# Kernel optimization log

Hardware: AMD Instinct MI355X
Metric: run time of the kernel (lower is better)

The kernel has to match this reference:

```python
import jax, jax.numpy as jnp
import numpy as np

B, S, D = 2, 2048, 2048
H, KV, HD = 32, 8, 64          # n_heads, n_kv_heads, head_dim
NREP = H // KV                 # GQA repeat factor
ROPE_THETA = 500000.0          # llama3 base


def setup_inputs() -> dict:
    key = jax.random.key(0)
    ks = jax.random.split(key, 5)
    scale = 1.0 / np.sqrt(D)
    x = jax.random.normal(ks[0], (B, S, D), dtype=jnp.float32)
    wq = jax.random.normal(ks[1], (D, H * HD), dtype=jnp.float32) * scale
    wk = jax.random.normal(ks[2], (D, KV * HD), dtype=jnp.float32) * scale
    wv = jax.random.normal(ks[3], (D, KV * HD), dtype=jnp.float32) * scale
    wo = jax.random.normal(ks[4], (H * HD, D), dtype=jnp.float32) * scale
    # real rotary freqs, matching precompute_freqs_cis: angle[t, j] = t / theta^(2j/HD)
    inv_freq = 1.0 / (ROPE_THETA ** (np.arange(0, HD, 2, dtype=np.float32) / HD))
    t = np.arange(S, dtype=np.float32)
    ang = np.outer(t, inv_freq)  # (S, HD//2)
    freqs_cos = jnp.asarray(np.cos(ang), dtype=jnp.float32)
    freqs_sin = jnp.asarray(np.sin(ang), dtype=jnp.float32)
    return {"x": x, "wq": wq, "wk": wk, "wv": wv, "wo": wo,
            "freqs_cos": freqs_cos, "freqs_sin": freqs_sin}


def _apply_rope(t, cos, sin):
    # t: (B, S, nh, HD); pairs (even, odd) = (real, imag) of complex number
    tr = t.reshape(*t.shape[:-1], HD // 2, 2)
    re, im = tr[..., 0], tr[..., 1]
    c = cos[None, :, None, :]   # (1, S, 1, HD//2)
    s = sin[None, :, None, :]
    out_re = re * c - im * s
    out_im = re * s + im * c
    return jnp.stack([out_re, out_im], axis=-1).reshape(t.shape)


def reference(x, wq, wk, wv, wo, freqs_cos, freqs_sin):
    bsz, seq_len, _ = x.shape
    xq = (x @ wq).reshape(bsz, seq_len, H, HD)
    xk = (x @ wk).reshape(bsz, seq_len, KV, HD)
    xv = (x @ wv).reshape(bsz, seq_len, KV, HD)
    xq = _apply_rope(xq, freqs_cos, freqs_sin)
    xk = _apply_rope(xk, freqs_cos, freqs_sin)
    # GQA without materializing repeated KV: group query heads by KV head
    q = xq.transpose(0, 2, 1, 3).reshape(bsz, KV, NREP, seq_len, HD)  # bgrqh
    k = xk.transpose(0, 2, 1, 3)                                      # bgkh over seq k
    v = xv.transpose(0, 2, 1, 3)
    scores = jnp.einsum("bgrqh,bgkh->bgrqk", q, k) / jnp.sqrt(jnp.float32(HD))
    causal = jnp.tril(jnp.ones((seq_len, seq_len), dtype=bool))
    scores = jnp.where(causal[None, None, None], scores, -jnp.inf)
    probs = jax.nn.softmax(scores.astype(jnp.float32), axis=-1).astype(q.dtype)
    out = jnp.einsum("bgrqk,bgkh->bgrqh", probs, v)
    out = out.reshape(bsz, H, seq_len, HD).transpose(0, 2, 1, 3).reshape(bsz, seq_len, H * HD)
    return out @ wo
```

## Files before the change

kernel.cpp:

```cpp
#include <hip/hip_runtime.h>
#include <hip/hip_bf16.h>

typedef __attribute__((ext_vector_type(8))) short bf16x8;
typedef __attribute__((ext_vector_type(4))) float f32x4;
typedef __attribute__((ext_vector_type(16))) float f32x16;

#define S_LEN 2048
#define DMODEL 2048
#define NH 32
#define NKV 8
#define HDIM 64
#define NQKV 3072
#define BROWS 4096
#define LOG2E 1.4426950408889634f

__device__ __forceinline__ float bf2f(unsigned short u) {
    union { unsigned int i; float f; } v; v.i = ((unsigned int)u) << 16; return v.f;
}
__device__ __forceinline__ unsigned short f2bf(float f) {
    union { float f; unsigned int i; } v; v.f = f;
    unsigned int r = v.i + 0x7fffu + ((v.i >> 16) & 1u);
    return (unsigned short)(r >> 16);
}

__device__ __forceinline__ unsigned cvtpk_bf16(float lo, float hi) {
    unsigned r;
    asm("v_cvt_pk_bf16_f32 %0, %1, %2" : "=v"(r) : "v"(lo), "v"(hi));
    return r;
}
__device__ __forceinline__ void pl32swap(unsigned &a, unsigned &b) {
    asm("v_permlane32_swap_b32 %0, %1" : "+v"(a), "+v"(b));
}
__device__ __forceinline__ float exp2_fast(float x) {
    float r;
    asm("v_exp_f32 %0, %1" : "=v"(r) : "v"(x));
    return r;
}

__device__ __forceinline__ void gload_lds16(const void* g, void* l) {
    __builtin_amdgcn_global_load_lds(
        (const __attribute__((address_space(1))) unsigned int*)(unsigned long long)g,
        (__attribute__((address_space(3))) unsigned int*)(unsigned int)(unsigned long long)l,
        16, 0, 0);
}

#define VMW(n) asm volatile("s_waitcnt vmcnt(" #n ")" ::: "memory")
#define CFENCE() asm volatile("" ::: "memory")

__global__ void cast_x_kernel(const float* __restrict__ x, unsigned short* __restrict__ xb) {
    int idx = blockIdx.x * blockDim.x + threadIdx.x;
    float4 v = ((const float4*)x)[idx];
    ushort4 o;
    o.x = f2bf(v.x); o.y = f2bf(v.y); o.z = f2bf(v.z); o.w = f2bf(v.w);
    ((ushort4*)xb)[idx] = o;
}

__global__ void tcast_kernel(const float* __restrict__ src, unsigned short* __restrict__ dst,
                             int K, int N) {
    __shared__ float t[32][33];
    int n0 = blockIdx.x * 32, k0 = blockIdx.y * 32;
    int tx = threadIdx.x & 31, ty = threadIdx.x >> 5;
#pragma unroll
    for (int i = 0; i < 32; i += 8)
        t[ty + i][tx] = src[(size_t)(k0 + ty + i) * N + n0 + tx];
    __syncthreads();
#pragma unroll
    for (int i = 0; i < 32; i += 8)
        dst[(size_t)(n0 + ty + i) * K + k0 + tx] = f2bf(t[tx][ty + i]);
}

__global__ void vtrans_kernel(const unsigned short* __restrict__ qkv,
                              unsigned short* __restrict__ vt) {
    __shared__ unsigned short t[32][33];
    int s0 = blockIdx.x * 32;
    int hd0 = (blockIdx.y & 1) * 32;
    int bg = blockIdx.y >> 1;
    int b = bg >> 3, g = bg & 7;
    int tx = threadIdx.x & 31, ty = threadIdx.x >> 5;
#pragma unroll
    for (int i = 0; i < 32; i += 8)
        t[ty + i][tx] = qkv[(size_t)(b * S_LEN + s0 + ty + i) * NQKV + 2560 + g * 64 + hd0 + tx];
    __syncthreads();
#pragma unroll
    for (int i = 0; i < 32; i += 8)
        vt[(size_t)(bg * 64 + hd0 + ty + i) * S_LEN + s0 + tx] = t[tx][ty + i];
}

template <int NJF, int OUTF32>
__global__ __launch_bounds__(512, 2) void gemm_wide_kernel(
    const unsigned short* __restrict__ A,
    const unsigned short* __restrict__ BT,
    void* __restrict__ Cv,
    int M, int N, int K, int nbx) {
    extern __shared__ __align__(16) unsigned short lds[];
    const int ABUF = 8192;
    const int BSTRIDE = NJF * 4096;
    const int BBASE = 2 * ABUF;

    const int nwg = gridDim.x;
    const int cpx = nwg >> 3;
    const int swz = ((int)blockIdx.x & 7) * cpx + ((int)blockIdx.x >> 3);
    const int m0 = (swz / nbx) * 128, n0 = (swz % nbx) * (NJF * 64);

    const int tid = threadIdx.x;
    const int lane = tid & 63, wid = tid >> 6;
    const int wr = wid >> 2, wc = wid & 3;
    const int l16 = lane & 15, lg = lane >> 4;

    const int sr0 = tid >> 3, sk0 = tid & 7;
    const int kc = (sk0 ^ (sr0 & 7)) * 8;
    const size_t K64 = (size_t)64 * K;
    const unsigned short* gA = A + (size_t)(m0 + sr0) * K + kc;
    const unsigned short* gB = BT + (size_t)(n0 + sr0) * K + kc;
    unsigned short* ldsA = lds + tid * 8;
    unsigned short* ldsB = lds + BBASE + tid * 8;

    f32x4 acc[4][NJF];
#pragma unroll
    for (int i = 0; i < 4; ++i)
#pragma unroll
        for (int j = 0; j < NJF; ++j)
#pragma unroll
            for (int e = 0; e < 4; ++e) acc[i][j][e] = 0.f;

    const int NT = K >> 6;
    {
        gload_lds16(gA, ldsA);
        gload_lds16(gA + K64, ldsA + 4096);
#pragma unroll
        for (int j = 0; j < NJF; ++j)
            gload_lds16(gB + (size_t)j * K64, ldsB + j * 4096);
    }

    for (int t = 0; t < NT; ++t) {
        const int cur = t & 1, nxt = cur ^ 1;
        if (t + 1 < NT) {
            gload_lds16(gA + 64, ldsA + nxt * ABUF);
            gload_lds16(gA + 64 + K64, ldsA + nxt * ABUF + 4096);
#pragma unroll
            for (int j = 0; j < NJF; ++j)
                gload_lds16(gB + 64 + (size_t)j * K64, ldsB + nxt * BSTRIDE + j * 4096);
            if constexpr (NJF == 6) { VMW(8); } else { VMW(6); }
        } else {
            VMW(0);
        }
        __builtin_amdgcn_s_barrier();
        CFENCE();

#pragma unroll
        for (int ks = 0; ks < 2; ++ks) {
            bf16x8 af[4], bfv[NJF];
#pragma unroll
            for (int mi = 0; mi < 4; ++mi) {
                const int rA = wr * 64 + mi * 16 + l16;
                af[mi] = *(const bf16x8*)(lds + cur * ABUF + rA * 64 + ((ks * 4 + lg) ^ (rA & 7)) * 8);
            }
#pragma unroll
            for (int nj = 0; nj < NJF; ++nj) {
                const int rB = nj * 64 + wc * 16 + l16;
                bfv[nj] = *(const bf16x8*)(lds + BBASE + cur * BSTRIDE + rB * 64 + ((ks * 4 + lg) ^ (rB & 7)) * 8);
            }
#pragma unroll
            for (int mi = 0; mi < 4; ++mi)
#pragma unroll
                for (int nj = 0; nj < NJF; ++nj)
                    acc[mi][nj] = __builtin_amdgcn_mfma_f32_16x16x32_bf16(
                        af[mi], bfv[nj], acc[mi][nj], 0, 0, 0);
        }
        CFENCE();
        __builtin_amdgcn_s_barrier();
        CFENCE();
        gA += 64;
        gB += 64;
    }

#pragma unroll
    for (int mi = 0; mi < 4; ++mi) {
        const int row = m0 + wr * 64 + mi * 16 + lg * 4;
#pragma unroll
        for (int e = 0; e < 4; ++e) {
            if (OUTF32) {
                float* Cf = (float*)Cv;
#pragma unroll
                for (int nj = 0; nj < NJF; ++nj)
                    Cf[(size_t)(row + e) * N + n0 + nj * 64 + wc * 16 + l16] = acc[mi][nj][e];
            } else {
                unsigned short* Cb = (unsigned short*)Cv;
#pragma unroll
                for (int nj = 0; nj < NJF; ++nj)
                    Cb[(size_t)(row + e) * N + n0 + nj * 64 + wc * 16 + l16] = f2bf(acc[mi][nj][e]);
            }
        }
    }
}

template <int OUTF32>
__global__ __launch_bounds__(256) void gemm_bt_kernel(
    const unsigned short* __restrict__ A,
    const unsigned short* __restrict__ BT,
    void* __restrict__ Cv,
    int M, int N, int K) {
    __shared__ __align__(16) unsigned short Als[128 * 32];
    __shared__ __align__(16) unsigned short Bls[128 * 32];

    const int tid = threadIdx.x;
    const int lane = tid & 63;
    const int wid = tid >> 6;
    const int wr = wid >> 1, wc = wid & 1;
    const int l16 = lane & 15, lg = lane >> 4;
    const int m0 = blockIdx.y * 128, n0 = blockIdx.x * 128;

    f32x4 acc[4][4];
#pragma unroll
    for (int i = 0; i < 4; ++i)
#pragma unroll
        for (int j = 0; j < 4; ++j)
#pragma unroll
            for (int e = 0; e < 4; ++e) acc[i][j][e] = 0.f;

    const int f0 = tid, f1 = 256 + tid;
    const int ar0 = f0 >> 2, ac0 = (f0 & 3) * 8;
    const int ar1 = f1 >> 2, ac1 = (f1 & 3) * 8;
    const size_t Abase = (size_t)m0 * K;
    const size_t Bbase = (size_t)n0 * K;

    for (int k0 = 0; k0 < K; k0 += 32) {
        __syncthreads();
        gload_lds16(A + Abase + (size_t)ar0 * K + k0 + ac0, Als + f0 * 8);
        gload_lds16(A + Abase + (size_t)ar1 * K + k0 + ac1, Als + f1 * 8);
        gload_lds16(BT + Bbase + (size_t)ar0 * K + k0 + ac0, Bls + f0 * 8);
        gload_lds16(BT + Bbase + (size_t)ar1 * K + k0 + ac1, Bls + f1 * 8);
        __syncthreads();
        bf16x8 af[4], bfv[4];
#pragma unroll
        for (int i = 0; i < 4; ++i)
            af[i] = *(const bf16x8*)(Als + (wr * 64 + i * 16 + l16) * 32 + lg * 8);
#pragma unroll
        for (int j = 0; j < 4; ++j)
            bfv[j] = *(const bf16x8*)(Bls + (wc * 64 + j * 16 + l16) * 32 + lg * 8);
#pragma unroll
        for (int i = 0; i < 4; ++i)
#pragma unroll
            for (int j = 0; j < 4; ++j)
                acc[i][j] = __builtin_amdgcn_mfma_f32_16x16x32_bf16(af[i], bfv[j], acc[i][j], 0, 0, 0);
    }

    const int row_base = m0 + wr * 64 + lg * 4;
    const int col_base = n0 + wc * 64 + l16;
    if (OUTF32) {
        float* Cf = (float*)Cv;
#pragma unroll
        for (int i = 0; i < 4; ++i)
#pragma unroll
            for (int r = 0; r < 4; ++r)
#pragma unroll
                for (int j = 0; j < 4; ++j)
                    Cf[(size_t)(row_base + i * 16 + r) * N + col_base + j * 16] = acc[i][j][r];
    } else {
        unsigned short* Cb = (unsigned short*)Cv;
#pragma unroll
        for (int i = 0; i < 4; ++i)
#pragma unroll
            for (int r = 0; r < 4; ++r)
#pragma unroll
                for (int j = 0; j < 4; ++j)
                    Cb[(size_t)(row_base + i * 16 + r) * N + col_base + j * 16] = f2bf(acc[i][j][r]);
    }
}

__global__ void rope_kernel(unsigned short* __restrict__ qkv,
                            const float* __restrict__ fc, const float* __restrict__ fs) {
    const int PAIRS = 1280;
    int idx = blockIdx.x * blockDim.x + threadIdx.x;
    int row = idx / PAIRS;
    int w = idx - row * PAIRS;
    int s = row & (S_LEN - 1);
    int col = (w < 1024) ? (w * 2) : (2048 + (w - 1024) * 2);
    int f = (col & 63) >> 1;
    float c = fc[s * 32 + f], sn = fs[s * 32 + f];
    unsigned int* p = (unsigned int*)(qkv + (size_t)row * NQKV + col);
    unsigned int v = *p;
    float re = bf2f((unsigned short)(v & 0xffffu));
    float im = bf2f((unsigned short)(v >> 16));
    float oro = re * c - im * sn;
    float oim = re * sn + im * c;
    if (w < 1024) { oro *= 0.125f * LOG2E; oim *= 0.125f * LOG2E; }
    *p = (unsigned int)f2bf(oro) | ((unsigned int)f2bf(oim) << 16);
}

__global__ __launch_bounds__(256) void attn_kernel(
    const unsigned short* __restrict__ qkv,
    const unsigned short* __restrict__ vt,
    unsigned short* __restrict__ aout) {
    __shared__ __align__(16) unsigned short Kls[2][64 * 64];
    __shared__ __align__(16) unsigned short Vls[2][64 * 64];
    __shared__ float Fbuf[4][32];

    const int tid = threadIdx.x, lane = tid & 63, wid = tid >> 6;
    const int l31 = lane & 31, hi = lane >> 5;
    const int g = blockIdx.x, b = blockIdx.y;
    const int h = g * 4 + wid;

    const int srow = tid >> 3, schk = tid & 7;
    const int sc = schk ^ (srow & 7);
    const unsigned short* kgs = qkv + (size_t)(b * S_LEN + srow) * NQKV + 2048 + g * 64 + sc * 8;
    const unsigned short* vgs = vt + (size_t)((b * 8 + g) * 64 + srow) * S_LEN + sc * 8;
    const int dd = tid * 8;

    const int xr = l31 & 7;

    const int chunk = 63 - (int)blockIdx.z;
    const int q0 = chunk * 32;
    const int ntiles = (chunk >> 1) + 1;
    const int qg_row = q0 + l31;

    bf16x8 qf[4];
    {
        const unsigned short* qp =
            qkv + (size_t)(b * S_LEN + q0 + l31) * NQKV + h * HDIM + hi * 8;
#pragma unroll
        for (int s = 0; s < 4; ++s) qf[s] = *(const bf16x8*)(qp + s * 16);
    }

    float l_r = 0.f;
    f32x16 oacc0, oacc1;
#pragma unroll
    for (int r = 0; r < 16; ++r) { oacc0[r] = 0.f; oacc1[r] = 0.f; }

    gload_lds16(kgs, Kls[0] + dd);
    gload_lds16(kgs + (size_t)32 * NQKV, Kls[0] + dd + 2048);
    gload_lds16(vgs, Vls[0] + dd);
    gload_lds16(vgs + (size_t)32 * S_LEN, Vls[0] + dd + 2048);
    __syncthreads();

    for (int t = 0; t < ntiles; ++t) {
        const int kv0 = t * 64;
        if (t + 1 < ntiles) {
            const int nkv = kv0 + 64;
            unsigned short* kd = Kls[(t + 1) & 1] + dd;
            unsigned short* vd = Vls[(t + 1) & 1] + dd;
            gload_lds16(kgs + (size_t)nkv * NQKV, kd);
            gload_lds16(kgs + (size_t)(nkv + 32) * NQKV, kd + 2048);
            gload_lds16(vgs + nkv, vd);
            gload_lds16(vgs + (size_t)32 * S_LEN + nkv, vd + 2048);
        }
        const unsigned short* Kb = Kls[t & 1];
        const unsigned short* Vb = Vls[t & 1];

        f32x16 s0, s1;
#pragma unroll
        for (int r = 0; r < 16; ++r) { s0[r] = 0.f; s1[r] = 0.f; }
        __builtin_amdgcn_s_setprio(1);
#pragma unroll
        for (int s = 0; s < 4; ++s) {
            const int coff = ((s * 2 + hi) ^ xr) * 8;
            bf16x8 kf0 = *(const bf16x8*)(Kb + l31 * 64 + coff);
            bf16x8 kf1 = *(const bf16x8*)(Kb + (32 + l31) * 64 + coff);
            s0 = __builtin_amdgcn_mfma_f32_32x32x16_bf16(kf0, qf[s], s0, 0, 0, 0);
            s1 = __builtin_amdgcn_mfma_f32_32x32x16_bf16(kf1, qf[s], s1, 0, 0, 0);
        }
        __builtin_amdgcn_s_setprio(0);
        if (t == ntiles - 1) {
#pragma unroll
            for (int r = 0; r < 16; ++r) {
                int kvr = kv0 + (r & 3) + 8 * (r >> 2) + 4 * hi;
                if (kvr > qg_row) s0[r] = -3.0e38f;
                if (kvr + 32 > qg_row) s1[r] = -3.0e38f;
            }
        }
        float r0 = 0.f, r1 = 0.f, r2 = 0.f, r3 = 0.f;
#pragma unroll
        for (int r = 0; r < 16; r += 4) {
            s0[r + 0] = exp2_fast(s0[r + 0]); r0 += s0[r + 0];
            s0[r + 1] = exp2_fast(s0[r + 1]); r1 += s0[r + 1];
            s0[r + 2] = exp2_fast(s0[r + 2]); r2 += s0[r + 2];
            s0[r + 3] = exp2_fast(s0[r + 3]); r3 += s0[r + 3];
        }
#pragma unroll
        for (int r = 0; r < 16; r += 4) {
            s1[r + 0] = exp2_fast(s1[r + 0]); r0 += s1[r + 0];
            s1[r + 1] = exp2_fast(s1[r + 1]); r1 += s1[r + 1];
            s1[r + 2] = exp2_fast(s1[r + 2]); r2 += s1[r + 2];
            s1[r + 3] = exp2_fast(s1[r + 3]); r3 += s1[r + 3];
        }
        l_r += (r0 + r1) + (r2 + r3);

        unsigned pw[4][4];
#define BUILD_PA(c, S, base)                                    \
        {                                                       \
            unsigned x0 = cvtpk_bf16(S[base + 0], S[base + 1]); \
            unsigned y0 = cvtpk_bf16(S[base + 4], S[base + 5]); \
            pl32swap(x0, y0);                                   \
            unsigned x1 = cvtpk_bf16(S[base + 2], S[base + 3]); \
            unsigned y1 = cvtpk_bf16(S[base + 6], S[base + 7]); \
            pl32swap(x1, y1);                                   \
            pw[c][0] = x0; pw[c][1] = x1; pw[c][2] = y0; pw[c][3] = y1; \
        }
        BUILD_PA(0, s0, 0)
        BUILD_PA(1, s0, 8)
        BUILD_PA(2, s1, 0)
        BUILD_PA(3, s1, 8)
#undef BUILD_PA

        __builtin_amdgcn_s_setprio(1);
#pragma unroll
        for (int c = 0; c < 4; ++c) {
            union { unsigned u[4]; bf16x8 v; } pa;
            pa.u[0] = pw[c][0]; pa.u[1] = pw[c][1]; pa.u[2] = pw[c][2]; pa.u[3] = pw[c][3];
            const int coff = ((c * 2 + hi) ^ xr) * 8;
            bf16x8 vf0 = *(const bf16x8*)(Vb + l31 * 64 + coff);
            bf16x8 vf1 = *(const bf16x8*)(Vb + (32 + l31) * 64 + coff);
            oacc0 = __builtin_amdgcn_mfma_f32_32x32x16_bf16(pa.v, vf0, oacc0, 0, 0, 0);
            oacc1 = __builtin_amdgcn_mfma_f32_32x32x16_bf16(pa.v, vf1, oacc1, 0, 0, 0);
        }
        __builtin_amdgcn_s_setprio(0);
        __syncthreads();
    }

    l_r += __shfl_xor(l_r, 32);
    if (lane < 32) Fbuf[wid][l31] = 1.0f / l_r;
    asm volatile("s_waitcnt lgkmcnt(0)" ::: "memory");
#pragma unroll
    for (int rg = 0; rg < 4; ++rg) {
#pragma unroll
        for (int rr = 0; rr < 4; ++rr) {
            int row = 8 * rg + 4 * hi + rr;
            float inv = Fbuf[wid][row];
            int r = rg * 4 + rr;
            size_t orow = (size_t)(b * S_LEN + q0 + row) * DMODEL + h * HDIM;
            aout[orow + l31] = f2bf(oacc0[r] * inv);
            aout[orow + 32 + l31] = f2bf(oacc1[r] * inv);
        }
    }
}

extern "C" void kernel_launch(void* const* d_in, const int* in_sizes, int n_in,
                              void* d_out, int out_size, void* d_ws, size_t ws_size,
                              hipStream_t stream) {
    const float* x = (const float*)d_in[0];
    const float* wq = (const float*)d_in[1];
    const float* wk = (const float*)d_in[2];
    const float* wv = (const float*)d_in[3];
    const float* wo = (const float*)d_in[4];
    const float* fc = (const float*)d_in[5];
    const float* fs = (const float*)d_in[6];
    float* out = (float*)d_out;

    unsigned short* xb = (unsigned short*)d_ws;
    unsigned short* wqkvT = xb + (size_t)BROWS * DMODEL;
    unsigned short* woT = wqkvT + (size_t)NQKV * DMODEL;
    unsigned short* qkvb = woT + (size_t)DMODEL * DMODEL;
    unsigned short* aoutb = xb;
    unsigned short* vtb = wqkvT;

    hipError_t e1 = hipFuncSetAttribute(
        reinterpret_cast<const void*>(&gemm_wide_kernel<6, 0>),
        hipFuncAttributeMaxDynamicSharedMemorySize, 131072);
    hipError_t e2 = hipFuncSetAttribute(
        reinterpret_cast<const void*>(&gemm_wide_kernel<4, 1>),
        hipFuncAttributeMaxDynamicSharedMemorySize, 98304);
    const bool big = (e1 == hipSuccess && e2 == hipSuccess);

    cast_x_kernel<<<(BROWS * DMODEL / 4) / 256, 256, 0, stream>>>(x, xb);
    tcast_kernel<<<dim3(DMODEL / 32, DMODEL / 32), 256, 0, stream>>>(wq, wqkvT, DMODEL, DMODEL);
    tcast_kernel<<<dim3(512 / 32, DMODEL / 32), 256, 0, stream>>>(wk, wqkvT + (size_t)2048 * DMODEL, DMODEL, 512);
    tcast_kernel<<<dim3(512 / 32, DMODEL / 32), 256, 0, stream>>>(wv, wqkvT + (size_t)2560 * DMODEL, DMODEL, 512);
    tcast_kernel<<<dim3(DMODEL / 32, DMODEL / 32), 256, 0, stream>>>(wo, woT, DMODEL, DMODEL);
    if (big)
        gemm_wide_kernel<6, 0><<<(BROWS / 128) * (NQKV / 384), 512, 131072, stream>>>(
            xb, wqkvT, qkvb, BROWS, NQKV, DMODEL, NQKV / 384);
    else
        gemm_bt_kernel<0><<<dim3(NQKV / 128, BROWS / 128), 256, 0, stream>>>(
            xb, wqkvT, qkvb, BROWS, NQKV, DMODEL);
    rope_kernel<<<(BROWS * 1280) / 256, 256, 0, stream>>>(qkvb, fc, fs);
    vtrans_kernel<<<dim3(S_LEN / 32, 32), 256, 0, stream>>>(qkvb, vtb);
    attn_kernel<<<dim3(NKV, 2, 64), 256, 0, stream>>>(qkvb, vtb, aoutb);
    if (big)
        gemm_wide_kernel<4, 1><<<(BROWS / 128) * (DMODEL / 256), 512, 98304, stream>>>(
            aoutb, woT, out, BROWS, DMODEL, DMODEL, DMODEL / 256);
    else
        gemm_bt_kernel<1><<<dim3(DMODEL / 128, BROWS / 128), 256, 0, stream>>>(
            aoutb, woT, out, BROWS, DMODEL, DMODEL);
}
```

Baseline: 179.8 us.

## Deepen GEMM pipeline to four-stage K=32 LDS ring buffer

Replaces the double-buffered K=64 tile loop in the wide GEMM with a four-slot ring of K=32 tiles, loading three stages ahead and using graded vmcnt waits at the tail. The LDS swizzle is changed to match 32-wide rows. The aim is to hide more global-load latency behind MFMA work. In exchange there are twice as many barriers per unit of K and less MFMA work between them, and the LDS footprint stays the same.

Result: slower. 184.6 us (+2.7%).

```diff
diff --git a/kernel.cpp b/kernel.cpp
--- a/kernel.cpp
+++ b/kernel.cpp
@@ -87,15 +87,14 @@
 }
 
 template <int NJF, int OUTF32>
-__global__ __launch_bounds__(512, 2) void gemm_wide_kernel(
+__global__ __launch_bounds__(512, 2) void gemm_deep_kernel(
     const unsigned short* __restrict__ A,
     const unsigned short* __restrict__ BT,
     void* __restrict__ Cv,
     int M, int N, int K, int nbx) {
     extern __shared__ __align__(16) unsigned short lds[];
-    const int ABUF = 8192;
-    const int BSTRIDE = NJF * 4096;
-    const int BBASE = 2 * ABUF;
+    constexpr int BUFS = 4096 + NJF * 2048;
+    constexpr int NBL = NJF / 2;
 
     const int nwg = gridDim.x;
     const int cpx = nwg >> 3;
@@ -107,13 +106,22 @@
     const int wr = wid >> 2, wc = wid & 3;
     const int l16 = lane & 15, lg = lane >> 4;
 
-    const int sr0 = tid >> 3, sk0 = tid & 7;
-    const int kc = (sk0 ^ (sr0 & 7)) * 8;
-    const size_t K64 = (size_t)64 * K;
-    const unsigned short* gA = A + (size_t)(m0 + sr0) * K + kc;
-    const unsigned short* gB = BT + (size_t)(n0 + sr0) * K + kc;
-    unsigned short* ldsA = lds + tid * 8;
-    unsigned short* ldsB = lds + BBASE + tid * 8;
+    const int sr = tid >> 2, sk = tid & 3;
+    const int kc = (sk ^ ((sr >> 1) & 3)) * 8;
+    const size_t K128 = (size_t)128 * K;
+    const unsigned short* gA = A + (size_t)(m0 + sr) * K + kc;
+    const unsigned short* gB = BT + (size_t)(n0 + sr) * K + kc;
+
+#define DSTAGE(T) do { \
+    const int _b = (T) & 3; \
+    gload_lds16(gA + (size_t)(T) * 32, lds + _b * BUFS + tid * 8); \
+    _Pragma("unroll") for (int j = 0; j < NBL; ++j) \
+        gload_lds16(gB + (size_t)(T) * 32 + (size_t)j * K128, \
+                    lds + _b * BUFS + 4096 + j * 4096 + tid * 8); \
+} while (0)
+#define VMW_3L() do { if constexpr (NJF == 6) { VMW(12); } else { VMW(9); } } while (0)
+#define VMW_2L() do { if constexpr (NJF == 6) { VMW(8); } else { VMW(6); } } while (0)
+#define VMW_1L() do { if constexpr (NJF == 6) { VMW(4); } else { VMW(3); } } while (0)
 
     f32x4 acc[4][NJF];
 #pragma unroll
@@ -123,55 +131,38 @@
 #pragma unroll
             for (int e = 0; e < 4; ++e) acc[i][j][e] = 0.f;
 
-    const int NT = K >> 6;
-    {
-        gload_lds16(gA, ldsA);
-        gload_lds16(gA + K64, ldsA + 4096);
-#pragma unroll
-        for (int j = 0; j < NJF; ++j)
-            gload_lds16(gB + (size_t)j * K64, ldsB + j * 4096);
-    }
+    const int NT = K >> 5;
+    DSTAGE(0); DSTAGE(1); DSTAGE(2);
 
     for (int t = 0; t < NT; ++t) {
-        const int cur = t & 1, nxt = cur ^ 1;
-        if (t + 1 < NT) {
-            gload_lds16(gA + 64, ldsA + nxt * ABUF);
-            gload_lds16(gA + 64 + K64, ldsA + nxt * ABUF + 4096);
-#pragma unroll
-            for (int j = 0; j < NJF; ++j)
-                gload_lds16(gB + 64 + (size_t)j * K64, ldsB + nxt * BSTRIDE + j * 4096);
-            if constexpr (NJF == 6) { VMW(8); } else { VMW(6); }
-        } else {
-            VMW(0);
-        }
+        if (t + 3 < NT) { DSTAGE(t + 3); VMW_3L(); }
+        else if (t + 2 < NT) { VMW_2L(); }
+        else if (t + 1 < NT) { VMW_1L(); }
+        else { VMW(0); }
         __builtin_amdgcn_s_barrier();
         CFENCE();
 
-#pragma unroll
-        for (int ks = 0; ks < 2; ++ks) {
-            bf16x8 af[4], bfv[NJF];
-#pragma unroll
-            for (int mi = 0; mi < 4; ++mi) {
-                const int rA = wr * 64 + mi * 16 + l16;
-                af[mi] = *(const bf16x8*)(lds + cur * ABUF + rA * 64 + ((ks * 4 + lg) ^ (rA & 7)) * 8);
-            }
-#pragma unroll
-            for (int nj = 0; nj < NJF; ++nj) {
-                const int rB = nj * 64 + wc * 16 + l16;
-                bfv[nj] = *(const bf16x8*)(lds + BBASE + cur * BSTRIDE + rB * 64 + ((ks * 4 + lg) ^ (rB & 7)) * 8);
-            }
-#pragma unroll
-            for (int mi = 0; mi < 4; ++mi)
-#pragma unroll
-                for (int nj = 0; nj < NJF; ++nj)
-                    acc[mi][nj] = __builtin_amdgcn_mfma_f32_16x16x32_bf16(
-                        af[mi], bfv[nj], acc[mi][nj], 0, 0, 0);
-        }
+        const unsigned short* bufp = lds + (t & 3) * BUFS;
+        bf16x8 af[4], bfv[NJF];
+#pragma unroll
+        for (int mi = 0; mi < 4; ++mi) {
+            const int rA = wr * 64 + mi * 16 + l16;
+            af[mi] = *(const bf16x8*)(bufp + rA * 32 + ((lg ^ ((rA >> 1) & 3)) * 8));
+        }
+#pragma unroll
+        for (int nj = 0; nj < NJF; ++nj) {
+            const int rB = nj * 64 + wc * 16 + l16;
+            bfv[nj] = *(const bf16x8*)(bufp + 4096 + rB * 32 + ((lg ^ ((rB >> 1) & 3)) * 8));
+        }
+#pragma unroll
+        for (int mi = 0; mi < 4; ++mi)
+#pragma unroll
+            for (int nj = 0; nj < NJF; ++nj)
+                acc[mi][nj] = __builtin_amdgcn_mfma_f32_16x16x32_bf16(
+                    af[mi], bfv[nj], acc[mi][nj], 0, 0, 0);
         CFENCE();
         __builtin_amdgcn_s_barrier();
         CFENCE();
-        gA += 64;
-        gB += 64;
     }
 
 #pragma unroll
@@ -192,6 +183,10 @@
             }
         }
     }
+#undef DSTAGE
+#undef VMW_3L
+#undef VMW_2L
+#undef VMW_1L
 }
 
 template <int OUTF32>
@@ -454,10 +449,10 @@
     unsigned short* vtb = wqkvT;
 
     hipError_t e1 = hipFuncSetAttribute(
-        reinterpret_cast<const void*>(&gemm_wide_kernel<6, 0>),
+        reinterpret_cast<const void*>(&gemm_deep_kernel<6, 0>),
         hipFuncAttributeMaxDynamicSharedMemorySize, 131072);
     hipError_t e2 = hipFuncSetAttribute(
-        reinterpret_cast<const void*>(&gemm_wide_kernel<4, 1>),
+        reinterpret_cast<const void*>(&gemm_deep_kernel<4, 1>),
         hipFuncAttributeMaxDynamicSharedMemorySize, 98304);
     const bool big = (e1 == hipSuccess && e2 == hipSuccess);
 
@@ -467,7 +462,7 @@
     tcast_kernel<<<dim3(512 / 32, DMODEL / 32), 256, 0, stream>>>(wv, wqkvT + (size_t)2560 * DMODEL, DMODEL, 512);
     tcast_kernel<<<dim3(DMODEL / 32, DMODEL / 32), 256, 0, stream>>>(wo, woT, DMODEL, DMODEL);
     if (big)
-        gemm_wide_kernel<6, 0><<<(BROWS / 128) * (NQKV / 384), 512, 131072, stream>>>(
+        gemm_deep_kernel<6, 0><<<(BROWS / 128) * (NQKV / 384), 512, 131072, stream>>>(
             xb, wqkvT, qkvb, BROWS, NQKV, DMODEL, NQKV / 384);
     else
         gemm_bt_kernel<0><<<dim3(NQKV / 128, BROWS / 128), 256, 0, stream>>>(
@@ -476,7 +471,7 @@
     vtrans_kernel<<<dim3(S_LEN / 32, 32), 256, 0, stream>>>(qkvb, vtb);
     attn_kernel<<<dim3(NKV, 2, 64), 256, 0, stream>>>(qkvb, vtb, aoutb);
     if (big)
-        gemm_wide_kernel<4, 1><<<(BROWS / 128) * (DMODEL / 256), 512, 98304, stream>>>(
+        gemm_deep_kernel<4, 1><<<(BROWS / 128) * (DMODEL / 256), 512, 98304, stream>>>(
             aoutb, woT, out, BROWS, DMODEL, DMODEL, DMODEL / 256);
     else
         gemm_bt_kernel<1><<<dim3(DMODEL / 128, BROWS / 128), 256, 0, stream>>>(
```
